# Kernel optimization log

Hardware: AMD Instinct MI355X
Metric: run time of the kernel (lower is better)

Reference implementation:

```python
import jax, jax.numpy as jnp
import numpy as np

N = 50000
E = 800000
IN_CH = 128
HID = 16
HEADS = 8
OUT_CH = 64
NEG_SLOPE = 0.2


def _gat_conv(x, src, dst, W, a_src, a_dst, b, heads, ch):
    # x: [N, F_in]; W: [F_in, heads*ch]; a_src/a_dst: [heads, ch]; b: [heads*ch] or [ch]
    n = x.shape[0]
    h = (x @ W).reshape(n, heads, ch)                      # [N, H, C]
    s = jnp.einsum('nhc,hc->nh', h, a_src)                 # [N, H]
    d = jnp.einsum('nhc,hc->nh', h, a_dst)                 # [N, H]
    e = jax.nn.leaky_relu(s[src] + d[dst], NEG_SLOPE)      # [E, H]
    # numerically stable segment softmax over destination neighborhoods
    m = jax.ops.segment_max(e, dst, num_segments=n)        # [N, H]
    m = jnp.where(jnp.isfinite(m), m, 0.0)                 # guard isolated nodes
    w = jnp.exp(e - m[dst])                                # [E, H]
    z = jax.ops.segment_sum(w, dst, num_segments=n)        # [N, H]
    alpha = w / (z[dst] + 1e-16)                           # [E, H]
    msg = h[src] * alpha[:, :, None]                       # [E, H, C]
    out = jax.ops.segment_sum(msg, dst, num_segments=n)    # [N, H, C]
    return out.reshape(n, heads * ch) + b


def setup_inputs() -> dict:
    key = jax.random.key(0)
    ks = jax.random.split(key, 10)
    x = jax.random.normal(ks[0], (N, IN_CH), dtype=jnp.float32)
    edge_index = jax.random.randint(ks[1], (2, E), 0, N, dtype=jnp.int64)
    g1 = 1.0 / np.sqrt(IN_CH)
    g2 = 1.0 / np.sqrt(HEADS * HID)
    W1 = jax.random.normal(ks[2], (IN_CH, HEADS * HID), dtype=jnp.float32) * g1
    a_src1 = jax.random.normal(ks[3], (HEADS, HID), dtype=jnp.float32) * g2
    a_dst1 = jax.random.normal(ks[4], (HEADS, HID), dtype=jnp.float32) * g2
    b1 = jnp.zeros((HEADS * HID,), dtype=jnp.float32)
    W2 = jax.random.normal(ks[5], (HEADS * HID, OUT_CH), dtype=jnp.float32) * g2
    a_src2 = jax.random.normal(ks[6], (1, OUT_CH), dtype=jnp.float32) * (1.0 / np.sqrt(OUT_CH))
    a_dst2 = jax.random.normal(ks[7], (1, OUT_CH), dtype=jnp.float32) * (1.0 / np.sqrt(OUT_CH))
    b2 = jnp.zeros((OUT_CH,), dtype=jnp.float32)
    return {"x": x, "edge_index": edge_index,
            "W1": W1, "a_src1": a_src1, "a_dst1": a_dst1, "b1": b1,
            "W2": W2, "a_src2": a_src2, "a_dst2": a_dst2, "b2": b2}


def reference(x, edge_index, W1, a_src1, a_dst1, b1, W2, a_src2, a_dst2, b2):
    src, dst = edge_index[0], edge_index[1]
    # dropout layers are identity at inference
    h = _gat_conv(x, src, dst, W1, a_src1, a_dst1, b1, HEADS, HID)
    h = jax.nn.elu(h)
    out = _gat_conv(h, src, dst, W2, a_src2, a_dst2, b2, 1, OUT_CH)
    return out
```

## Files before the change

### kernel.cpp

```cpp
#include <hip/hip_runtime.h>
#include <hip/hip_fp16.h>

#define INCH   128
#define HEADS1 8
#define HID1   16
#define C1     128
#define C2     64
#define NEG_SLOPE 0.2f
#define SB     256

using f16x8 = __attribute__((ext_vector_type(8))) _Float16;
using f32x4 = __attribute__((ext_vector_type(4))) float;

__device__ __forceinline__ float lrelu(float v) { return v >= 0.f ? v : NEG_SLOPE * v; }
__device__ __forceinline__ int swzA(int row, int byteInRow) {
  return (row << 8) | (byteInRow ^ ((row & 15) << 4));
}

__global__ void prep_kernel(const float* __restrict__ x, __half* __restrict__ xh,
                            const float* __restrict__ W1, __half* __restrict__ W1t,
                            const float* __restrict__ W2, __half* __restrict__ W2t,
                            const float* __restrict__ a_src1, const float* __restrict__ a_dst1,
                            const float* __restrict__ a_src2, const float* __restrict__ a_dst2,
                            __half* __restrict__ B1e, __half* __restrict__ B2e,
                            const int* __restrict__ dst, int* __restrict__ deg,
                            int cvtB, int tB, int total8, int E) {
  const int b = blockIdx.x, t = threadIdx.x;
  if (b < cvtB) {
    int i = b * 256 + t;
    if (i >= total8) return;
    const float4* p = (const float4*)x + (size_t)i * 2;
    float4 v0 = p[0], v1 = p[1];
    __half2 ha = __floats2half2_rn(v0.x, v0.y);
    __half2 hb = __floats2half2_rn(v0.z, v0.w);
    __half2 hc = __floats2half2_rn(v1.x, v1.y);
    __half2 hd = __floats2half2_rn(v1.z, v1.w);
    uint4 w = { *(unsigned*)&ha, *(unsigned*)&hb, *(unsigned*)&hc, *(unsigned*)&hd };
    ((uint4*)xh)[i] = w;
  } else if (b < cvtB + tB) {
    int id = (b - cvtB) * 256 + t;
    if (id < 16384) {
      int col = id >> 7, k = id & 127;
      W1t[id] = __float2half(W1[k * 128 + col]);
    } else if (id < 24576) {
      int idx = id - 16384;
      int col = idx >> 7, k = idx & 127;
      W2t[idx] = __float2half(W2[k * 64 + col]);
    } else if (id < 26624) {
      int idx = id - 24576;
      int col = idx >> 7, k = idx & 127;
      const float* av = (col < 8) ? a_src1 : a_dst1;
      int hh = col & 7;
      float s = 0.f;
#pragma unroll
      for (int c = 0; c < 16; ++c) s += W1[k * 128 + hh * 16 + c] * av[hh * 16 + c];
      B1e[col * 128 + k] = __float2half(s);
    } else if (id < 28672) {
      int idx = id - 26624;
      int col = idx >> 7, k = idx & 127;
      float s = 0.f;
      if (col == 0) {
#pragma unroll
        for (int c = 0; c < 64; ++c) s += W2[k * 64 + c] * a_src2[c];
      } else if (col == 1) {
#pragma unroll
        for (int c = 0; c < 64; ++c) s += W2[k * 64 + c] * a_dst2[c];
      }
      B2e[col * 128 + k] = __float2half(s);
    }
  } else {
    int e = (b - cvtB - tB) * 256 + t;
    if (e < E) atomicAdd(&deg[dst[e]], 1);
  }
}


__global__ void scan1_kernel(const int* __restrict__ deg, int* __restrict__ partial,
                             int* __restrict__ cursor, int N) {
  __shared__ int sh[SB];
  const int b = blockIdx.x, t = threadIdx.x;
  const int chunk = (N + SB - 1) / SB;
  const int lo = b * chunk, hi = min(lo + chunk, N);
  int s = 0;
  for (int i = lo + t; i < hi; i += SB) {
    s += deg[i];
    cursor[i] = 0;
  }
  sh[t] = s;
  __syncthreads();
  for (int off = SB / 2; off; off >>= 1) {
    if (t < off) sh[t] += sh[t + off];
    __syncthreads();
  }
  if (t == 0) partial[b] = sh[0];
}

__global__ void scan3_kernel(const int* __restrict__ deg, const int* __restrict__ partial,
                             int* __restrict__ row_start, int N) {
  __shared__ int pref[SB];
  __shared__ int sh[SB];
  const int b = blockIdx.x, t = threadIdx.x;
  int pv = partial[t];
  pref[t] = pv;
  __syncthreads();
  for (int off = 1; off < SB; off <<= 1) {
    int u = (t >= off) ? pref[t - off] : 0;
    __syncthreads();
    pref[t] += u;
    __syncthreads();
  }
  const int chunk = (N + SB - 1) / SB;
  const int lo = b * chunk, hi = min(lo + chunk, N);
  int run = (b == 0) ? 0 : pref[b - 1];
  for (int base = lo; base < hi; base += SB) {
    int i = base + t;
    int v = (i < hi) ? deg[i] : 0;
    sh[t] = v;
    __syncthreads();
    for (int off = 1; off < SB; off <<= 1) {
      int u = (t >= off) ? sh[t - off] : 0;
      __syncthreads();
      sh[t] += u;
      __syncthreads();
    }
    if (i < hi) row_start[i] = run + sh[t] - v;
    run += sh[SB - 1];
    __syncthreads();
  }
  if (b == SB - 1 && t == 0) row_start[N] = run;
}

__global__ void fill_kernel(const int* __restrict__ src, const int* __restrict__ dst,
                            const int* __restrict__ row_start, int* __restrict__ cursor,
                            int* __restrict__ src_sorted, int E) {
  int e = blockIdx.x * blockDim.x + threadIdx.x;
  if (e >= E) return;
  int d = dst[e];
  int slot = row_start[d] + atomicAdd(&cursor[d], 1);
  src_sorted[slot] = src[e];
}

__global__ __launch_bounds__(256) void gemm1_mfma(
    const __half* __restrict__ xh, const __half* __restrict__ W1t,
    const __half* __restrict__ B1e,
    __half* __restrict__ h1, float* __restrict__ s1, float* __restrict__ d1, int M) {
  __shared__ unsigned char As[16384];
  __shared__ unsigned char Bs[36864];
  const int t = threadIdx.x;
  const int m0 = blockIdx.x * 64;
  for (int c = t; c < 1024; c += 256) {
    int row = c >> 4, seg = c & 15;
    int gr = m0 + row;
    uint4 v = make_uint4(0, 0, 0, 0);
    if (gr < M) v = ((const uint4*)xh)[(unsigned)(gr << 4) + seg];
    *(uint4*)(As + swzA(row, seg << 4)) = v;
  }
  for (int c = t; c < 2304; c += 256) {
    int row = c >> 4, seg = c & 15;
    if (row < 128) {
      uint4 v = ((const uint4*)W1t)[(row << 4) + seg];
      *(uint4*)(Bs + swzA(row, seg << 4)) = v;
    } else {
      uint4 v = ((const uint4*)B1e)[((row - 128) << 4) + seg];
      *(uint4*)(Bs + 32768 + swzA(row - 128, seg << 4)) = v;
    }
  }
  __syncthreads();
  const int l = t & 63, wid = t >> 6;
  const int c16 = l & 15;
  const int kOff = (l >> 4) << 4;
  const int rA = (wid << 4) | c16;
  f16x8 a[4];
#pragma unroll
  for (int kb = 0; kb < 4; ++kb)
    a[kb] = *(const f16x8*)(As + swzA(rA, (kb << 6) + kOff));
#pragma unroll
  for (int ct = 0; ct < 9; ++ct) {
    const unsigned char* bbase = (ct < 8) ? Bs : (Bs + 32768);
    const int rB = (ct < 8) ? ((ct << 4) | c16) : c16;
    f32x4 acc = {0.f, 0.f, 0.f, 0.f};
#pragma unroll
    for (int kb = 0; kb < 4; ++kb) {
      f16x8 b = *(const f16x8*)(bbase + swzA(rB, (kb << 6) + kOff));
      acc = __builtin_amdgcn_mfma_f32_16x16x32_f16(a[kb], b, acc, 0, 0, 0);
    }
    if (ct < 8) {
      const int colg = (ct << 4) + c16;
#pragma unroll
      for (int i = 0; i < 4; ++i) {
        const int n = m0 + (wid << 4) + ((l >> 4) << 2) + i;
        if (n < M) h1[(unsigned)(n << 7) + colg] = __float2half(acc[i]);
      }
    } else {
#pragma unroll
      for (int i = 0; i < 4; ++i) {
        const int n = m0 + (wid << 4) + ((l >> 4) << 2) + i;
        if (n < M) {
          if (c16 < 8) s1[n * HEADS1 + c16] = acc[i];
          else         d1[n * HEADS1 + (c16 - 8)] = acc[i];
        }
      }
    }
  }
}

__global__ __launch_bounds__(256) void gemm2_mfma(
    const __half* __restrict__ x2h, const __half* __restrict__ W2t,
    const __half* __restrict__ B2e,
    __half* __restrict__ h2, float* __restrict__ s2, float* __restrict__ d2, int M) {
  __shared__ unsigned char As[16384];
  __shared__ unsigned char Bs[20480];
  const int t = threadIdx.x;
  const int m0 = blockIdx.x * 64;
  for (int c = t; c < 1024; c += 256) {
    int row = c >> 4, seg = c & 15;
    int gr = m0 + row;
    uint4 v = make_uint4(0, 0, 0, 0);
    if (gr < M) v = ((const uint4*)x2h)[(unsigned)(gr << 4) + seg];
    *(uint4*)(As + swzA(row, seg << 4)) = v;
  }
  for (int c = t; c < 1280; c += 256) {
    int row = c >> 4, seg = c & 15;
    if (row < 64) {
      uint4 v = ((const uint4*)W2t)[(row << 4) + seg];
      *(uint4*)(Bs + swzA(row, seg << 4)) = v;
    } else {
      uint4 v = ((const uint4*)B2e)[((row - 64) << 4) + seg];
      *(uint4*)(Bs + 16384 + swzA(row - 64, seg << 4)) = v;
    }
  }
  __syncthreads();
  const int l = t & 63, wid = t >> 6;
  const int c16 = l & 15;
  const int kOff = (l >> 4) << 4;
  const int rA = (wid << 4) | c16;
  f16x8 a[4];
#pragma unroll
  for (int kb = 0; kb < 4; ++kb)
    a[kb] = *(const f16x8*)(As + swzA(rA, (kb << 6) + kOff));
#pragma unroll
  for (int ct = 0; ct < 5; ++ct) {
    const unsigned char* bbase = (ct < 4) ? Bs : (Bs + 16384);
    const int rB = (ct < 4) ? ((ct << 4) | c16) : c16;
    f32x4 acc = {0.f, 0.f, 0.f, 0.f};
#pragma unroll
    for (int kb = 0; kb < 4; ++kb) {
      f16x8 b = *(const f16x8*)(bbase + swzA(rB, (kb << 6) + kOff));
      acc = __builtin_amdgcn_mfma_f32_16x16x32_f16(a[kb], b, acc, 0, 0, 0);
    }
    if (ct < 4) {
      const int colg = (ct << 4) + c16;
#pragma unroll
      for (int i = 0; i < 4; ++i) {
        const int n = m0 + (wid << 4) + ((l >> 4) << 2) + i;
        if (n < M) h2[(unsigned)(n << 6) + colg] = __float2half(acc[i]);
      }
    } else {
#pragma unroll
      for (int i = 0; i < 4; ++i) {
        const int n = m0 + (wid << 4) + ((l >> 4) << 2) + i;
        if (n < M) {
          if (c16 == 0) s2[n] = acc[i];
          else if (c16 == 1) d2[n] = acc[i];
        }
      }
    }
  }
}

__global__ __launch_bounds__(256) void layer1_agg(
    const int* __restrict__ row_start, const int* __restrict__ src_sorted,
    const float* __restrict__ s1, const float* __restrict__ d1,
    const __half* __restrict__ h1, const float* __restrict__ b1,
    __half* __restrict__ x2h, int N) {
  __shared__ float wlds[4][64][8];
  const int wv = threadIdx.x >> 6;
  const int lane = threadIdx.x & 63;
  const int le = lane >> 3, h = lane & 7;
  const int es = lane >> 4, cl = lane & 15;
  const int hh = cl >> 1;
  const uint4* __restrict__ h1v = (const uint4*)h1;
  const int waveId = blockIdx.x * 4 + wv;
  const int stride = gridDim.x * 4;
  for (int n = waveId; n < N; n += stride) {
    const int lo = row_start[n], hi = row_start[n + 1];
    const float dv = d1[n * HEADS1 + h];
    float z = 0.f;
    float acc[8] = {0.f, 0.f, 0.f, 0.f, 0.f, 0.f, 0.f, 0.f};
    for (int base = lo; base < hi; base += 64) {
      const int cnt = min(64, hi - base);
      const int c1 = cnt - 1;
      const int j0 = le, j1 = 8 + le;
      const int sj0 = src_sorted[base + min(j0, c1)];
      const int sj1 = src_sorted[base + min(j1, c1)];
      const float sv0 = s1[sj0 * HEADS1 + h];
      const float sv1 = s1[sj1 * HEADS1 + h];
      const int ps0 = src_sorted[base + min(es, c1)];
      const int ps1 = src_sorted[base + min(4 + es, c1)];
      const int ps2 = src_sorted[base + min(8 + es, c1)];
      const int ps3 = src_sorted[base + min(12 + es, c1)];
      const uint4 pf0 = h1v[(unsigned)(ps0 << 4) + cl];
      const uint4 pf1 = h1v[(unsigned)(ps1 << 4) + cl];
      const uint4 pf2 = h1v[(unsigned)(ps2 << 4) + cl];
      const uint4 pf3 = h1v[(unsigned)(ps3 << 4) + cl];
      const float w0 = (j0 < cnt) ? __expf(lrelu(sv0 + dv)) : 0.f;
      const float w1 = (j1 < cnt) ? __expf(lrelu(sv1 + dv)) : 0.f;
      z += w0 + w1;
      const int rmax = (cnt + 7) >> 3;
      for (int r = 2; r < rmax; ++r) {
        const int j = (r << 3) + le;
        float w = 0.f;
        if (j < cnt) w = __expf(lrelu(s1[src_sorted[base + j] * HEADS1 + h] + dv));
        wlds[wv][j][h] = w;
        z += w;
      }
      {
        const float wA = __shfl(w0, (es << 3) | hh);
        const float wB = __shfl(w0, ((4 + es) << 3) | hh);
        const __half2* pA = (const __half2*)&pf0;
        const __half2* pB = (const __half2*)&pf1;
#pragma unroll
        for (int k = 0; k < 4; ++k) {
          float2 a2 = __half22float2(pA[k]);
          float2 b2v = __half22float2(pB[k]);
          acc[2 * k]     += wA * a2.x + wB * b2v.x;
          acc[2 * k + 1] += wA * a2.y + wB * b2v.y;
        }
      }
      if (cnt > 8) {
        const float wA = __shfl(w1, (es << 3) | hh);
        const float wB = __shfl(w1, ((4 + es) << 3) | hh);
        const __half2* pA = (const __half2*)&pf2;
        const __half2* pB = (const __half2*)&pf3;
#pragma unroll
        for (int k = 0; k < 4; ++k) {
          float2 a2 = __half22float2(pA[k]);
          float2 b2v = __half22float2(pB[k]);
          acc[2 * k]     += wA * a2.x + wB * b2v.x;
          acc[2 * k + 1] += wA * a2.y + wB * b2v.y;
        }
      }
      for (int i = 16; i < cnt; i += 8) {
        const int jA = i + es, jB = i + 4 + es;
        const float wA = wlds[wv][jA][hh];
        const float wB = wlds[wv][jB][hh];
        const int sA = src_sorted[base + min(jA, c1)];
        const int sB = src_sorted[base + min(jB, c1)];
        const uint4 fA = h1v[(unsigned)(sA << 4) + cl];
        const uint4 fB = h1v[(unsigned)(sB << 4) + cl];
        const __half2* pA = (const __half2*)&fA;
        const __half2* pB = (const __half2*)&fB;
#pragma unroll
        for (int k = 0; k < 4; ++k) {
          float2 a2 = __half22float2(pA[k]);
          float2 b2v = __half22float2(pB[k]);
          acc[2 * k]     += wA * a2.x + wB * b2v.x;
          acc[2 * k + 1] += wA * a2.y + wB * b2v.y;
        }
      }
    }
    z += __shfl_xor(z, 8); z += __shfl_xor(z, 16); z += __shfl_xor(z, 32);
    const float zsel = __shfl(z, hh);
#pragma unroll
    for (int k = 0; k < 8; ++k) {
      acc[k] += __shfl_xor(acc[k], 16);
      acc[k] += __shfl_xor(acc[k], 32);
    }
    if (es == 0) {
      const float zinv = 1.f / (zsel + 1e-16f);
      __half2 o[4];
#pragma unroll
      for (int k = 0; k < 4; ++k) {
        float ox = acc[2 * k] * zinv + b1[(cl << 3) + 2 * k];
        float oy = acc[2 * k + 1] * zinv + b1[(cl << 3) + 2 * k + 1];
        ox = ox > 0.f ? ox : expm1f(ox);
        oy = oy > 0.f ? oy : expm1f(oy);
        o[k] = __floats2half2_rn(ox, oy);
      }
      ((uint4*)x2h)[(unsigned)(n << 4) + cl] = *(const uint4*)o;
    }
  }
}

__global__ __launch_bounds__(256) void layer2_agg(
    const int* __restrict__ row_start, const int* __restrict__ src_sorted,
    const float* __restrict__ s2, const float* __restrict__ d2,
    const __half* __restrict__ h2, const float* __restrict__ b2,
    float* __restrict__ out, int N) {
  const int wv = threadIdx.x >> 6;
  const int lane = threadIdx.x & 63;
  const int es = lane >> 3, cl = lane & 7;
  const uint4* __restrict__ h2v = (const uint4*)h2;
  const int waveId = blockIdx.x * 4 + wv;
  const int stride = gridDim.x * 4;
  for (int n = waveId; n < N; n += stride) {
    const int lo = row_start[n], hi = row_start[n + 1];
    const float dv = d2[n];
    float z = 0.f;
    float acc[8] = {0.f, 0.f, 0.f, 0.f, 0.f, 0.f, 0.f, 0.f};
    for (int base = lo; base < hi; base += 64) {
      const int cnt = min(64, hi - base);
      const int c1 = cnt - 1;
      const int sidx = src_sorted[base + min(lane, c1)];
      const float sval = s2[sidx];
      const int ps0 = src_sorted[base + min(es, c1)];
      const int ps1 = src_sorted[base + min(8 + es, c1)];
      const int ps2 = src_sorted[base + min(16 + es, c1)];
      const int ps3 = src_sorted[base + min(24 + es, c1)];
      const uint4 pf0 = h2v[(unsigned)(ps0 << 3) + cl];
      const uint4 pf1 = h2v[(unsigned)(ps1 << 3) + cl];
      const uint4 pf2 = h2v[(unsigned)(ps2 << 3) + cl];
      const uint4 pf3 = h2v[(unsigned)(ps3 << 3) + cl];
      const float w = (lane < cnt) ? __expf(lrelu(sval + dv)) : 0.f;
      z += w;
      {
        const float wA = __shfl(w, es);
        const float wB = __shfl(w, 8 + es);
        const __half2* pA = (const __half2*)&pf0;
        const __half2* pB = (const __half2*)&pf1;
#pragma unroll
        for (int k = 0; k < 4; ++k) {
          float2 a2 = __half22float2(pA[k]);
          float2 b2v = __half22float2(pB[k]);
          acc[2 * k]     += wA * a2.x + wB * b2v.x;
          acc[2 * k + 1] += wA * a2.y + wB * b2v.y;
        }
      }
      if (cnt > 16) {
        const float wA = __shfl(w, 16 + es);
        const float wB = __shfl(w, 24 + es);
        const __half2* pA = (const __half2*)&pf2;
        const __half2* pB = (const __half2*)&pf3;
#pragma unroll
        for (int k = 0; k < 4; ++k) {
          float2 a2 = __half22float2(pA[k]);
          float2 b2v = __half22float2(pB[k]);
          acc[2 * k]     += wA * a2.x + wB * b2v.x;
          acc[2 * k + 1] += wA * a2.y + wB * b2v.y;
        }
      }
      for (int i = 32; i < cnt; i += 16) {
        const int jA = i + es, jB = i + 8 + es;
        const float wA = __shfl(w, jA);
        const float wB = __shfl(w, jB);
        const int sA = src_sorted[base + min(jA, c1)];
        const int sB = src_sorted[base + min(jB, c1)];
        const uint4 fA = h2v[(unsigned)(sA << 3) + cl];
        const uint4 fB = h2v[(unsigned)(sB << 3) + cl];
        const __half2* pA = (const __half2*)&fA;
        const __half2* pB = (const __half2*)&fB;
#pragma unroll
        for (int k = 0; k < 4; ++k) {
          float2 a2 = __half22float2(pA[k]);
          float2 b2v = __half22float2(pB[k]);
          acc[2 * k]     += wA * a2.x + wB * b2v.x;
          acc[2 * k + 1] += wA * a2.y + wB * b2v.y;
        }
      }
    }
#pragma unroll
    for (int off = 1; off < 64; off <<= 1) z += __shfl_xor(z, off);
#pragma unroll
    for (int k = 0; k < 8; ++k) {
      acc[k] += __shfl_xor(acc[k], 8);
      acc[k] += __shfl_xor(acc[k], 16);
      acc[k] += __shfl_xor(acc[k], 32);
    }
    if (es == 0) {
      const float zinv = 1.f / (z + 1e-16f);
      float4 o0, o1;
      o0.x = acc[0] * zinv + b2[(cl << 3) + 0];
      o0.y = acc[1] * zinv + b2[(cl << 3) + 1];
      o0.z = acc[2] * zinv + b2[(cl << 3) + 2];
      o0.w = acc[3] * zinv + b2[(cl << 3) + 3];
      o1.x = acc[4] * zinv + b2[(cl << 3) + 4];
      o1.y = acc[5] * zinv + b2[(cl << 3) + 5];
      o1.z = acc[6] * zinv + b2[(cl << 3) + 6];
      o1.w = acc[7] * zinv + b2[(cl << 3) + 7];
      float4* po = (float4*)&out[(unsigned)(n << 6) + (cl << 3)];
      po[0] = o0;
      po[1] = o1;
    }
  }
}

extern "C" void kernel_launch(void* const* d_in, const int* in_sizes, int n_in,
                              void* d_out, int out_size, void* d_ws, size_t ws_size,
                              hipStream_t stream) {
  const float* x      = (const float*)d_in[0];
  const int*   ei     = (const int*)d_in[1];
  const float* W1     = (const float*)d_in[2];
  const float* a_src1 = (const float*)d_in[3];
  const float* a_dst1 = (const float*)d_in[4];
  const float* b1     = (const float*)d_in[5];
  const float* W2     = (const float*)d_in[6];
  const float* a_src2 = (const float*)d_in[7];
  const float* a_dst2 = (const float*)d_in[8];
  const float* b2     = (const float*)d_in[9];
  float* out = (float*)d_out;

  const int N = in_sizes[0] / INCH;
  const int E = in_sizes[1] / 2;
  const int* src = ei;
  const int* dst = ei + E;

  float* ws = (float*)d_ws;
  size_t o = 0;
  __half* xh  = (__half*)(ws + o); o += (size_t)N * C1 / 2;
  __half* h1  = (__half*)(ws + o); o += (size_t)N * C1 / 2;
  __half* x2h = (__half*)(ws + o); o += (size_t)N * C1 / 2;
  float*  s1  = ws + o;            o += (size_t)N * HEADS1;
  float*  d1  = ws + o;            o += (size_t)N * HEADS1;
  __half* W1t = (__half*)(ws + o); o += 128 * 128 / 2;
  __half* W2t = (__half*)(ws + o); o += 64 * 128 / 2;
  __half* B1e = (__half*)(ws + o); o += 16 * 128 / 2;
  __half* B2e = (__half*)(ws + o); o += 16 * 128 / 2;
  int* deg        = (int*)(ws + o); o += N;
  int* cursor     = (int*)(ws + o); o += N;
  int* row_start  = (int*)(ws + o); o += N + 1;
  int* partial    = (int*)(ws + o); o += SB;
  int* src_sorted = (int*)(ws + o); o += E;
  __half* h2 = h1;
  float*  s2 = (float*)h1 + (size_t)N * 32;
  float*  d2 = s2 + N;

  const int EB = (E + 255) / 256;
  const int NB64 = (N + 63) / 64;
  const int total8 = N * C1 / 8;
  const int cvtB = (total8 + 255) / 256;
  const int tB = (16384 + 8192 + 2048 + 2048) / 256;
  const int histB = EB;
  const int AGGB = min((N + 3) / 4, 2048);

  hipMemsetAsync(deg, 0, (size_t)N * 4, stream);

  prep_kernel<<<cvtB + tB + histB, 256, 0, stream>>>(
      x, xh, W1, W1t, W2, W2t, a_src1, a_dst1, a_src2, a_dst2, B1e, B2e,
      dst, deg, cvtB, tB, total8, E);
  scan1_kernel<<<SB, SB, 0, stream>>>(deg, partial, cursor, N);
  scan3_kernel<<<SB, SB, 0, stream>>>(deg, partial, row_start, N);
  fill_kernel<<<EB, 256, 0, stream>>>(src, dst, row_start, cursor, src_sorted, E);

  gemm1_mfma<<<NB64, 256, 0, stream>>>(xh, W1t, B1e, h1, s1, d1, N);
  layer1_agg<<<AGGB, 256, 0, stream>>>(row_start, src_sorted, s1, d1, h1, b1, x2h, N);

  gemm2_mfma<<<NB64, 256, 0, stream>>>(x2h, W2t, B2e, h2, s2, d2, N);
  layer2_agg<<<AGGB, 256, 0, stream>>>(row_start, src_sorted, s2, d2, h2, b2, out, N);
}
```

Before: 186.4 us.

## Software-pipeline next node's row bounds and attention scores in aggregation kernels

Both aggregation kernels now prefetch the next node's row_start bounds, the first source attention scores, and the destination score while the current node is still being processed. The grid-stride loop is restructured so the first 64-edge chunk is handled specially and any further chunks go through a separate tail loop. The aim is to hide the dependent-load latency chain (row_start, then src, then s) that each wave used to stall on at the start of every node. The cost is higher register pressure and more code complexity, which may reduce occupancy.

```diff
diff --git a/kernel.cpp b/kernel.cpp
--- a/kernel.cpp
+++ b/kernel.cpp
@@ -282,38 +282,65 @@
   const uint4* __restrict__ h1v = (const uint4*)h1;
   const int waveId = blockIdx.x * 4 + wv;
   const int stride = gridDim.x * 4;
-  for (int n = waveId; n < N; n += stride) {
-    const int lo = row_start[n], hi = row_start[n + 1];
-    const float dv = d1[n * HEADS1 + h];
+
+  int n = waveId;
+  if (n >= N) return;
+  int lo = row_start[n], hi = row_start[n + 1];
+  float sv0 = 0.f, sv1 = 0.f, dvv;
+  {
+    const int cnt = min(64, hi - lo);
+    if (cnt > 0) {
+      const int c1 = cnt - 1;
+      const int sj0 = src_sorted[lo + min(le, c1)];
+      const int sj1 = src_sorted[lo + min(8 + le, c1)];
+      sv0 = s1[sj0 * HEADS1 + h];
+      sv1 = s1[sj1 * HEADS1 + h];
+    }
+    dvv = d1[n * HEADS1 + h];
+  }
+  while (true) {
+    const int n2 = n + stride;
+    int lo2 = 0, hi2 = 0;
+    if (n2 < N) { lo2 = row_start[n2]; hi2 = row_start[n2 + 1]; }
+    const int cnt = min(64, hi - lo);
+    const int c1 = cnt - 1;
     float z = 0.f;
     float acc[8] = {0.f, 0.f, 0.f, 0.f, 0.f, 0.f, 0.f, 0.f};
-    for (int base = lo; base < hi; base += 64) {
-      const int cnt = min(64, hi - base);
-      const int c1 = cnt - 1;
-      const int j0 = le, j1 = 8 + le;
-      const int sj0 = src_sorted[base + min(j0, c1)];
-      const int sj1 = src_sorted[base + min(j1, c1)];
-      const float sv0 = s1[sj0 * HEADS1 + h];
-      const float sv1 = s1[sj1 * HEADS1 + h];
-      const int ps0 = src_sorted[base + min(es, c1)];
-      const int ps1 = src_sorted[base + min(4 + es, c1)];
-      const int ps2 = src_sorted[base + min(8 + es, c1)];
-      const int ps3 = src_sorted[base + min(12 + es, c1)];
-      const uint4 pf0 = h1v[(unsigned)(ps0 << 4) + cl];
-      const uint4 pf1 = h1v[(unsigned)(ps1 << 4) + cl];
-      const uint4 pf2 = h1v[(unsigned)(ps2 << 4) + cl];
-      const uint4 pf3 = h1v[(unsigned)(ps3 << 4) + cl];
-      const float w0 = (j0 < cnt) ? __expf(lrelu(sv0 + dv)) : 0.f;
-      const float w1 = (j1 < cnt) ? __expf(lrelu(sv1 + dv)) : 0.f;
-      z += w0 + w1;
-      const int rmax = (cnt + 7) >> 3;
-      for (int r = 2; r < rmax; ++r) {
-        const int j = (r << 3) + le;
-        float w = 0.f;
-        if (j < cnt) w = __expf(lrelu(s1[src_sorted[base + j] * HEADS1 + h] + dv));
-        wlds[wv][j][h] = w;
-        z += w;
-      }
+    uint4 pf0, pf1, pf2, pf3;
+    if (cnt > 0) {
+      const int ps0 = src_sorted[lo + min(es, c1)];
+      const int ps1 = src_sorted[lo + min(4 + es, c1)];
+      const int ps2 = src_sorted[lo + min(8 + es, c1)];
+      const int ps3 = src_sorted[lo + min(12 + es, c1)];
+      pf0 = h1v[(unsigned)(ps0 << 4) + cl];
+      pf1 = h1v[(unsigned)(ps1 << 4) + cl];
+      pf2 = h1v[(unsigned)(ps2 << 4) + cl];
+      pf3 = h1v[(unsigned)(ps3 << 4) + cl];
+    }
+    const float w0 = (le < cnt) ? __expf(lrelu(sv0 + dvv)) : 0.f;
+    const float w1 = (8 + le < cnt) ? __expf(lrelu(sv1 + dvv)) : 0.f;
+    z += w0 + w1;
+    float nsv0 = 0.f, nsv1 = 0.f, ndv = 0.f;
+    if (n2 < N) {
+      const int cnt2 = min(64, hi2 - lo2);
+      if (cnt2 > 0) {
+        const int c12 = cnt2 - 1;
+        const int a0 = src_sorted[lo2 + min(le, c12)];
+        const int a1 = src_sorted[lo2 + min(8 + le, c12)];
+        nsv0 = s1[a0 * HEADS1 + h];
+        nsv1 = s1[a1 * HEADS1 + h];
+      }
+      ndv = d1[n2 * HEADS1 + h];
+    }
+    const int rmax = (cnt + 7) >> 3;
+    for (int r = 2; r < rmax; ++r) {
+      const int j = (r << 3) + le;
+      float w = 0.f;
+      if (j < cnt) w = __expf(lrelu(s1[src_sorted[lo + j] * HEADS1 + h] + dvv));
+      wlds[wv][j][h] = w;
+      z += w;
+    }
+    if (cnt > 0) {
       {
         const float wA = __shfl(w0, (es << 3) | hh);
         const float wB = __shfl(w0, ((4 + es) << 3) | hh);
@@ -344,8 +371,38 @@
         const int jA = i + es, jB = i + 4 + es;
         const float wA = wlds[wv][jA][hh];
         const float wB = wlds[wv][jB][hh];
-        const int sA = src_sorted[base + min(jA, c1)];
-        const int sB = src_sorted[base + min(jB, c1)];
+        const int sA = src_sorted[lo + min(jA, c1)];
+        const int sB = src_sorted[lo + min(jB, c1)];
+        const uint4 fA = h1v[(unsigned)(sA << 4) + cl];
+        const uint4 fB = h1v[(unsigned)(sB << 4) + cl];
+        const __half2* pA = (const __half2*)&fA;
+        const __half2* pB = (const __half2*)&fB;
+#pragma unroll
+        for (int k = 0; k < 4; ++k) {
+          float2 a2 = __half22float2(pA[k]);
+          float2 b2v = __half22float2(pB[k]);
+          acc[2 * k]     += wA * a2.x + wB * b2v.x;
+          acc[2 * k + 1] += wA * a2.y + wB * b2v.y;
+        }
+      }
+    }
+    for (int base = lo + 64; base < hi; base += 64) {
+      const int ccnt = min(64, hi - base);
+      const int cc1 = ccnt - 1;
+      const int rm2 = (ccnt + 7) >> 3;
+      for (int r = 0; r < rm2; ++r) {
+        const int j = (r << 3) + le;
+        float w = 0.f;
+        if (j < ccnt) w = __expf(lrelu(s1[src_sorted[base + j] * HEADS1 + h] + dvv));
+        wlds[wv][j][h] = w;
+        z += w;
+      }
+      for (int i = 0; i < ccnt; i += 8) {
+        const int jA = i + es, jB = i + 4 + es;
+        const float wA = wlds[wv][jA][hh];
+        const float wB = wlds[wv][jB][hh];
+        const int sA = src_sorted[base + min(jA, cc1)];
+        const int sB = src_sorted[base + min(jB, cc1)];
         const uint4 fA = h1v[(unsigned)(sA << 4) + cl];
         const uint4 fB = h1v[(unsigned)(sB << 4) + cl];
         const __half2* pA = (const __half2*)&fA;
@@ -379,6 +436,8 @@
       }
       ((uint4*)x2h)[(unsigned)(n << 4) + cl] = *(const uint4*)o;
     }
+    if (n2 >= N) break;
+    n = n2; lo = lo2; hi = hi2; sv0 = nsv0; sv1 = nsv1; dvv = ndv;
   }
 }
 
@@ -393,26 +452,52 @@
   const uint4* __restrict__ h2v = (const uint4*)h2;
   const int waveId = blockIdx.x * 4 + wv;
   const int stride = gridDim.x * 4;
-  for (int n = waveId; n < N; n += stride) {
-    const int lo = row_start[n], hi = row_start[n + 1];
-    const float dv = d2[n];
+
+  int n = waveId;
+  if (n >= N) return;
+  int lo = row_start[n], hi = row_start[n + 1];
+  float sval = 0.f, dvv;
+  {
+    const int cnt = min(64, hi - lo);
+    if (cnt > 0) {
+      const int c1 = cnt - 1;
+      const int s = src_sorted[lo + min(lane, c1)];
+      sval = s2[s];
+    }
+    dvv = d2[n];
+  }
+  while (true) {
+    const int n2 = n + stride;
+    int lo2 = 0, hi2 = 0;
+    if (n2 < N) { lo2 = row_start[n2]; hi2 = row_start[n2 + 1]; }
+    const int cnt = min(64, hi - lo);
+    const int c1 = cnt - 1;
     float z = 0.f;
     float acc[8] = {0.f, 0.f, 0.f, 0.f, 0.f, 0.f, 0.f, 0.f};
-    for (int base = lo; base < hi; base += 64) {
-      const int cnt = min(64, hi - base);
-      const int c1 = cnt - 1;
-      const int sidx = src_sorted[base + min(lane, c1)];
-      const float sval = s2[sidx];
-      const int ps0 = src_sorted[base + min(es, c1)];
-      const int ps1 = src_sorted[base + min(8 + es, c1)];
-      const int ps2 = src_sorted[base + min(16 + es, c1)];
-      const int ps3 = src_sorted[base + min(24 + es, c1)];
-      const uint4 pf0 = h2v[(unsigned)(ps0 << 3) + cl];
-      const uint4 pf1 = h2v[(unsigned)(ps1 << 3) + cl];
-      const uint4 pf2 = h2v[(unsigned)(ps2 << 3) + cl];
-      const uint4 pf3 = h2v[(unsigned)(ps3 << 3) + cl];
-      const float w = (lane < cnt) ? __expf(lrelu(sval + dv)) : 0.f;
-      z += w;
+    uint4 pf0, pf1, pf2, pf3;
+    if (cnt > 0) {
+      const int ps0 = src_sorted[lo + min(es, c1)];
+      const int ps1 = src_sorted[lo + min(8 + es, c1)];
+      const int ps2 = src_sorted[lo + min(16 + es, c1)];
+      const int ps3 = src_sorted[lo + min(24 + es, c1)];
+      pf0 = h2v[(unsigned)(ps0 << 3) + cl];
+      pf1 = h2v[(unsigned)(ps1 << 3) + cl];
+      pf2 = h2v[(unsigned)(ps2 << 3) + cl];
+      pf3 = h2v[(unsigned)(ps3 << 3) + cl];
+    }
+    const float w = (lane < cnt) ? __expf(lrelu(sval + dvv)) : 0.f;
+    z += w;
+    float nsval = 0.f, ndv = 0.f;
+    if (n2 < N) {
+      const int cnt2 = min(64, hi2 - lo2);
+      if (cnt2 > 0) {
+        const int c12 = cnt2 - 1;
+        const int s = src_sorted[lo2 + min(lane, c12)];
+        nsval = s2[s];
+      }
+      ndv = d2[n2];
+    }
+    if (cnt > 0) {
       {
         const float wA = __shfl(w, es);
         const float wB = __shfl(w, 8 + es);
@@ -443,8 +528,33 @@
         const int jA = i + es, jB = i + 8 + es;
         const float wA = __shfl(w, jA);
         const float wB = __shfl(w, jB);
-        const int sA = src_sorted[base + min(jA, c1)];
-        const int sB = src_sorted[base + min(jB, c1)];
+        const int sA = src_sorted[lo + min(jA, c1)];
+        const int sB = src_sorted[lo + min(jB, c1)];
+        const uint4 fA = h2v[(unsigned)(sA << 3) + cl];
+        const uint4 fB = h2v[(unsigned)(sB << 3) + cl];
+        const __half2* pA = (const __half2*)&fA;
+        const __half2* pB = (const __half2*)&fB;
+#pragma unroll
+        for (int k = 0; k < 4; ++k) {
+          float2 a2 = __half22float2(pA[k]);
+          float2 b2v = __half22float2(pB[k]);
+          acc[2 * k]     += wA * a2.x + wB * b2v.x;
+          acc[2 * k + 1] += wA * a2.y + wB * b2v.y;
+        }
+      }
+    }
+    for (int base = lo + 64; base < hi; base += 64) {
+      const int ccnt = min(64, hi - base);
+      const int cc1 = ccnt - 1;
+      float wc = 0.f;
+      if (lane < ccnt) wc = __expf(lrelu(s2[src_sorted[base + lane]] + dvv));
+      z += wc;
+      for (int i = 0; i < ccnt; i += 16) {
+        const int jA = i + es, jB = i + 8 + es;
+        const float wA = __shfl(wc, jA);
+        const float wB = __shfl(wc, jB);
+        const int sA = src_sorted[base + min(jA, cc1)];
+        const int sB = src_sorted[base + min(jB, cc1)];
         const uint4 fA = h2v[(unsigned)(sA << 3) + cl];
         const uint4 fB = h2v[(unsigned)(sB << 3) + cl];
         const __half2* pA = (const __half2*)&fA;
@@ -481,6 +591,8 @@
       po[0] = o0;
       po[1] = o1;
     }
+    if (n2 >= N) break;
+    n = n2; lo = lo2; hi = hi2; sval = nsval; dvv = ndv;
   }
 }
 
```

New measurement: 214.3 us. 1.15x slower.
